# Performance work log

Hardware: AMD Instinct MI355X
Metric: run time of the kernel (lower is better)

The kernel has to match this reference:

```python
import jax, jax.numpy as jnp
import numpy as np

S, H = 8192, 2048

def setup_inputs() -> dict:
    key = jax.random.key(0)
    k1, k2, k3 = jax.random.split(key, 3)
    hidden = jax.random.normal(k1, (1, H), dtype=jnp.float32)
    encoder_outputs = jax.random.normal(k2, (S, 1, H), dtype=jnp.float32)
    W = jax.random.normal(k3, (H, H), dtype=jnp.float32) * (1.0 / np.sqrt(H))
    b = jnp.zeros((H,), dtype=jnp.float32)
    return {"hidden": hidden, "encoder_outputs": encoder_outputs, "W": W, "b": b}

def reference(hidden, encoder_outputs, W, b):
    # hidden: [1, H] -> [H]; encoder_outputs: [S, 1, H] -> [S, H]
    h = hidden[0]                      # [H]
    enc = encoder_outputs[:, 0, :]     # [S, H]
    # method='general': energy_i = h . (W @ enc_i + b)
    proj = jnp.einsum('sh,kh->sk', enc, W) + b   # [S, H] (Linear: x @ W.T + b)
    energies = proj @ h                          # [S]
    attn = jax.nn.softmax(energies, axis=0)      # softmax over seq dim
    return attn[None, None, :]                   # [1, 1, S]
```

## Files before the change

kernel.cpp:

```cpp
#include <hip/hip_runtime.h>


#define Hdim 2048
#define Sdim 8192

typedef float vfloat4 __attribute__((ext_vector_type(4)));

__global__ void kv_matvec(const float* __restrict__ W, const float* __restrict__ hid,
                          float* __restrict__ v) {
    int b = blockIdx.x;
    int c0 = (b & 7) * 256 + (b >> 3) * 8;
    int t = threadIdx.x;
    int cp = (t & 1) * 4;
    int rl = t >> 1;
    float4 acc = {0.f, 0.f, 0.f, 0.f};
#pragma unroll
    for (int i = 0; i < 8; ++i) {
        int k = rl + 256 * i;
        float hk = hid[k];
        float4 w = *reinterpret_cast<const float4*>(W + (size_t)k * Hdim + c0 + cp);
        acc.x += w.x * hk;
        acc.y += w.y * hk;
        acc.z += w.z * hk;
        acc.w += w.w * hk;
    }
    __shared__ float4 red[512];
    red[t] = acc;
    __syncthreads();
    for (int s = 128; s > 0; s >>= 1) {
        if (rl < s) {
            float4 o = red[t + 2 * s];
            float4 m = red[t];
            m.x += o.x; m.y += o.y; m.z += o.z; m.w += o.w;
            red[t] = m;
        }
        __syncthreads();
    }
    if (t < 2) *reinterpret_cast<float4*>(v + c0 + t * 4) = red[t];
}

__global__ void k2_energies(const float* __restrict__ enc, const float* __restrict__ v,
                            float* __restrict__ e) {
    int t = threadIdx.x;
    int lane = t & 63;
    int s = blockIdx.x * 4 + (t >> 6);
    const float* row = enc + (size_t)s * Hdim;
    float acc = 0.f;
#pragma unroll
    for (int i = 0; i < 8; ++i) {
        int idx = i * 256 + lane * 4;
        vfloat4 a = __builtin_nontemporal_load(reinterpret_cast<const vfloat4*>(row + idx));
        float4 w = *reinterpret_cast<const float4*>(v + idx);
        acc += a.x * w.x + a.y * w.y + a.z * w.z + a.w * w.w;
    }
#pragma unroll
    for (int off = 32; off > 0; off >>= 1) acc += __shfl_xor(acc, off, 64);
    if (lane == 0) e[s] = acc;
}

__global__ void k3_softmax(const float* __restrict__ e, float* __restrict__ out) {
    __shared__ float red[16];
    __shared__ float bcast;
    int t = threadIdx.x;
    int lane = t & 63, wid = t >> 6;
    float4 a = *reinterpret_cast<const float4*>(e + t * 8);
    float4 bq = *reinterpret_cast<const float4*>(e + t * 8 + 4);
    float vals[8] = {a.x, a.y, a.z, a.w, bq.x, bq.y, bq.z, bq.w};
    float m = vals[0];
#pragma unroll
    for (int i = 1; i < 8; ++i) m = fmaxf(m, vals[i]);
#pragma unroll
    for (int off = 32; off > 0; off >>= 1) m = fmaxf(m, __shfl_xor(m, off, 64));
    if (lane == 0) red[wid] = m;
    __syncthreads();
    if (wid == 0) {
        float mm = (lane < 16) ? red[lane] : -1e30f;
#pragma unroll
        for (int off = 8; off > 0; off >>= 1) mm = fmaxf(mm, __shfl_xor(mm, off, 64));
        if (lane == 0) bcast = mm;
    }
    __syncthreads();
    m = bcast;
    float ex[8];
    float s = 0.f;
#pragma unroll
    for (int i = 0; i < 8; ++i) {
        ex[i] = __expf(vals[i] - m);
        s += ex[i];
    }
#pragma unroll
    for (int off = 32; off > 0; off >>= 1) s += __shfl_xor(s, off, 64);
    __syncthreads();
    if (lane == 0) red[wid] = s;
    __syncthreads();
    if (wid == 0) {
        float ss = (lane < 16) ? red[lane] : 0.f;
#pragma unroll
        for (int off = 8; off > 0; off >>= 1) ss += __shfl_xor(ss, off, 64);
        if (lane == 0) bcast = ss;
    }
    __syncthreads();
    float inv = 1.0f / bcast;
    float4 o1 = {ex[0] * inv, ex[1] * inv, ex[2] * inv, ex[3] * inv};
    float4 o2 = {ex[4] * inv, ex[5] * inv, ex[6] * inv, ex[7] * inv};
    *reinterpret_cast<float4*>(out + t * 8) = o1;
    *reinterpret_cast<float4*>(out + t * 8 + 4) = o2;
}

extern "C" void kernel_launch(void* const* d_in, const int* in_sizes, int n_in,
                              void* d_out, int out_size, void* d_ws, size_t ws_size,
                              hipStream_t stream) {
    const float* hid = (const float*)d_in[0];
    const float* enc = (const float*)d_in[1];
    const float* W   = (const float*)d_in[2];
    float* out = (float*)d_out;
    float* ws = (float*)d_ws;

    float* v = ws;
    float* e = v + Hdim;

    kv_matvec<<<256, 512, 0, stream>>>(W, hid, v);
    k2_energies<<<Sdim / 4, 256, 0, stream>>>(enc, v, e);
    k3_softmax<<<1, 1024, 0, stream>>>(e, out);
}
```

Measured before the change: 23.63 us.

## Split softmax into per-block partial max/sum and parallel normalize kernel

The energies kernel now also emits a per-block (max, sum-exp) pair over its four rows. The single-block softmax is replaced by a 32-block kernel in which every block re-reduces the 2048 pairs into the global max and sum, then normalizes its own slice of outputs. This moves the final softmax off one CU at the cost of redundant pair reductions per block and an extra syncthreads in the energies kernel. The nontemporal load hint on the encoder rows is also dropped in favour of a plain float4 load.

```diff
diff --git a/kernel.cpp b/kernel.cpp
--- a/kernel.cpp
+++ b/kernel.cpp
@@ -3,8 +3,7 @@
 
 #define Hdim 2048
 #define Sdim 8192
-
-typedef float vfloat4 __attribute__((ext_vector_type(4)));
+#define NBLK2 2048
 
 __global__ void kv_matvec(const float* __restrict__ W, const float* __restrict__ hid,
                           float* __restrict__ v) {
@@ -40,71 +39,68 @@
 }
 
 __global__ void k2_energies(const float* __restrict__ enc, const float* __restrict__ v,
-                            float* __restrict__ e) {
+                            float* __restrict__ e, float2* __restrict__ pairs) {
     int t = threadIdx.x;
     int lane = t & 63;
-    int s = blockIdx.x * 4 + (t >> 6);
+    int wave = t >> 6;
+    int s = blockIdx.x * 4 + wave;
     const float* row = enc + (size_t)s * Hdim;
     float acc = 0.f;
 #pragma unroll
     for (int i = 0; i < 8; ++i) {
         int idx = i * 256 + lane * 4;
-        vfloat4 a = __builtin_nontemporal_load(reinterpret_cast<const vfloat4*>(row + idx));
+        float4 a = *reinterpret_cast<const float4*>(row + idx);
         float4 w = *reinterpret_cast<const float4*>(v + idx);
         acc += a.x * w.x + a.y * w.y + a.z * w.z + a.w * w.w;
     }
 #pragma unroll
     for (int off = 32; off > 0; off >>= 1) acc += __shfl_xor(acc, off, 64);
-    if (lane == 0) e[s] = acc;
+    __shared__ float se[4];
+    if (lane == 0) {
+        e[s] = acc;
+        se[wave] = acc;
+    }
+    __syncthreads();
+    if (t == 0) {
+        float m = fmaxf(fmaxf(se[0], se[1]), fmaxf(se[2], se[3]));
+        float l = __expf(se[0] - m) + __expf(se[1] - m) + __expf(se[2] - m) + __expf(se[3] - m);
+        pairs[blockIdx.x] = make_float2(m, l);
+    }
 }
 
-__global__ void k3_softmax(const float* __restrict__ e, float* __restrict__ out) {
-    __shared__ float red[16];
-    __shared__ float bcast;
+__global__ void k3_norm(const float* __restrict__ e, const float2* __restrict__ pairs,
+                        float* __restrict__ out) {
     int t = threadIdx.x;
-    int lane = t & 63, wid = t >> 6;
-    float4 a = *reinterpret_cast<const float4*>(e + t * 8);
-    float4 bq = *reinterpret_cast<const float4*>(e + t * 8 + 4);
-    float vals[8] = {a.x, a.y, a.z, a.w, bq.x, bq.y, bq.z, bq.w};
-    float m = vals[0];
+    int lane = t & 63, wave = t >> 6;
+    float m = -1e30f;
+    float2 p[8];
 #pragma unroll
-    for (int i = 1; i < 8; ++i) m = fmaxf(m, vals[i]);
+    for (int j = 0; j < 8; ++j) {
+        p[j] = pairs[t + 256 * j];
+        m = fmaxf(m, p[j].x);
+    }
 #pragma unroll
     for (int off = 32; off > 0; off >>= 1) m = fmaxf(m, __shfl_xor(m, off, 64));
-    if (lane == 0) red[wid] = m;
+    __shared__ float red[4];
+    __shared__ float bcastM, bcastL;
+    if (lane == 0) red[wave] = m;
     __syncthreads();
-    if (wid == 0) {
-        float mm = (lane < 16) ? red[lane] : -1e30f;
+    if (t == 0) bcastM = fmaxf(fmaxf(red[0], red[1]), fmaxf(red[2], red[3]));
+    __syncthreads();
+    float M = bcastM;
+    float l = 0.f;
 #pragma unroll
-        for (int off = 8; off > 0; off >>= 1) mm = fmaxf(mm, __shfl_xor(mm, off, 64));
-        if (lane == 0) bcast = mm;
-    }
+    for (int j = 0; j < 8; ++j) l += p[j].y * __expf(p[j].x - M);
+#pragma unroll
+    for (int off = 32; off > 0; off >>= 1) l += __shfl_xor(l, off, 64);
     __syncthreads();
-    m = bcast;
-    float ex[8];
-    float s = 0.f;
-#pragma unroll
-    for (int i = 0; i < 8; ++i) {
-        ex[i] = __expf(vals[i] - m);
-        s += ex[i];
-    }
-#pragma unroll
-    for (int off = 32; off > 0; off >>= 1) s += __shfl_xor(s, off, 64);
+    if (lane == 0) red[wave] = l;
     __syncthreads();
-    if (lane == 0) red[wid] = s;
+    if (t == 0) bcastL = red[0] + red[1] + red[2] + red[3];
     __syncthreads();
-    if (wid == 0) {
-        float ss = (lane < 16) ? red[lane] : 0.f;
-#pragma unroll
-        for (int off = 8; off > 0; off >>= 1) ss += __shfl_xor(ss, off, 64);
-        if (lane == 0) bcast = ss;
-    }
-    __syncthreads();
-    float inv = 1.0f / bcast;
-    float4 o1 = {ex[0] * inv, ex[1] * inv, ex[2] * inv, ex[3] * inv};
-    float4 o2 = {ex[4] * inv, ex[5] * inv, ex[6] * inv, ex[7] * inv};
-    *reinterpret_cast<float4*>(out + t * 8) = o1;
-    *reinterpret_cast<float4*>(out + t * 8 + 4) = o2;
+    float invL = 1.0f / bcastL;
+    int idx = blockIdx.x * 256 + t;
+    out[idx] = __expf(e[idx] - M) * invL;
 }
 
 extern "C" void kernel_launch(void* const* d_in, const int* in_sizes, int n_in,
@@ -118,8 +114,9 @@
 
     float* v = ws;
     float* e = v + Hdim;
+    float2* pairs = (float2*)(e + Sdim);
 
     kv_matvec<<<256, 512, 0, stream>>>(W, hid, v);
-    k2_energies<<<Sdim / 4, 256, 0, stream>>>(enc, v, e);
-    k3_softmax<<<1, 1024, 0, stream>>>(e, out);
+    k2_energies<<<NBLK2, 256, 0, stream>>>(enc, v, e, pairs);
+    k3_norm<<<32, 256, 0, stream>>>(e, pairs, out);
 }
```

Measured after the change: 25.81 us. 1.09x slower.
